# Kernel optimization log

Measured on AMD Instinct MI355X. Metric: run time of the kernel, lower is better.

Reference implementation:

```python
import jax, jax.numpy as jnp
import numpy as np

EPS = 1e-5  # BatchNorm eps; fresh module eval => running_mean=0, running_var=1


def _cbr(t, W, g, b):
    # 1x1 conv (no bias) over [B,C,L] + BatchNorm2d(eval, mean0/var1) + ReLU
    t = jnp.einsum('oc,bcl->bol', W, t)
    t = t * (g / jnp.sqrt(1.0 + EPS))[None, :, None] + b[None, :, None]
    return jax.nn.relu(t)


def _wavelet(y):
    # SFP.wavelet: chunk channels into 3; for chunk i (1-based) take the level-i
    # haar wavedec approximation coeffs along axis 2 and mean-reduce them.
    # For even lengths, level-i haar approx = block-sum over 2^i samples * 2^(-i/2).
    B, C, L = y.shape
    parts = jnp.split(y, 3, axis=1)
    zs = []
    for i, k in enumerate(parts, start=1):
        s = 2 ** i
        a = k.reshape(B, C // 3, L // s, s).sum(-1) * (2.0 ** (-i / 2))  # [B,C/3,L/2^i]
        zs.append(a.mean(axis=2))
    return jnp.concatenate(zs, axis=1)  # [B,C]


def setup_inputs() -> dict:
    key = jax.random.key(0)
    ks = jax.random.split(key, 16)
    B, C, H, W = 32, 384, 64, 64
    R = C // 16
    f = lambda k, sh, s=0.05: jax.random.normal(k, sh, jnp.float32) * s
    u = lambda k, sh: jax.random.uniform(k, sh, jnp.float32, 0.5, 1.5)
    return dict(
        x=jax.random.normal(ks[0], (B, C, H, W), jnp.float32),
        Wy=f(ks[1], (C, C)), gy=u(ks[2], (C,)), by=f(ks[3], (C,)),
        Wh=f(ks[4], (C, C)), gh=u(ks[5], (C,)), bh=f(ks[6], (C,)),
        Ww=f(ks[7], (C, C)), gw=u(ks[8], (C,)), bw=f(ks[9], (C,)),
        fc0_w=f(ks[10], (R, C)), fc0_b=f(ks[11], (R,)),
        bn1_g=u(ks[12], (R,)), bn1_b=f(ks[13], (R,)),
        fc1_w=f(ks[14], (C, R)), fc1_b=f(ks[15], (C,)),
    )


def reference(x, Wy, gy, by, Wh, gh, bh, Ww, gw, bw,
              fc0_w, fc0_b, bn1_g, bn1_b, fc1_w, fc1_b):
    B, C, H, Wd = x.shape
    # CoordPooling: mean over width -> [B,C,H]; mean over height -> [B,C,W]; cat along coord axis
    y = jnp.concatenate([x.mean(axis=3), x.mean(axis=2)], axis=2)  # [B,C,H+W]
    y = _cbr(y, Wy, gy, by)
    xh = _cbr(y[:, :, :H], Wh, gh, bh)   # [B,C,H]
    xw = _cbr(y[:, :, H:], Ww, gw, bw)   # [B,C,W]
    # SFP channel gate (torch detaches y before the wavelet)
    z = _wavelet(jax.lax.stop_gradient(y))          # [B,C]
    z = z @ fc0_w.T + fc0_b                          # [B,C/16]
    z = jax.nn.relu(z * (bn1_g / jnp.sqrt(1.0 + EPS)) + bn1_b)
    z = z @ fc1_w.T + fc1_b                          # [B,C]
    gate = jax.nn.sigmoid(xh[:, :, :, None] * xw[:, :, None, :])  # [B,C,H,W]
    return x * gate + x * z[:, :, None, None]
```

## Files before the change

### kernel.cpp

```cpp
#include <hip/hip_runtime.h>
#include <math.h>

#define RSQ 0.99999500003749975f

typedef __attribute__((ext_vector_type(8))) __bf16 bf16x8;
typedef __attribute__((ext_vector_type(4))) float f32x4;
typedef __attribute__((ext_vector_type(4))) unsigned int u32x4;
typedef __attribute__((ext_vector_type(2))) unsigned int u32x2;

__device__ __forceinline__ unsigned short bfb(float v) {
    return __builtin_bit_cast(unsigned short, (__bf16)v);
}
__device__ __forceinline__ float bff(unsigned short u) {
    unsigned int x = ((unsigned int)u) << 16;
    return __builtin_bit_cast(float, x);
}

__global__ __launch_bounds__(256) void kpool(const float* __restrict__ x,
                                             const float* __restrict__ Wy,
                                             const float* __restrict__ Wh,
                                             const float* __restrict__ Ww,
                                             unsigned short* __restrict__ ypb,
                                             unsigned short* __restrict__ Wp) {
    __shared__ float sm[6208];
    int bid = blockIdx.x;
    int t = threadIdx.x;
    if (bid >= 12288) {
        int e = bid - 12288;
        int m = e / 24, ot = e % 24;
        const float* W = (m == 0) ? Wy : (m == 1) ? Wh : Ww;
#pragma unroll
        for (int k = 0; k < 6; ++k) {
            int idx = t + k * 256;
            int r = idx / 96, c4 = idx % 96;
            f32x4 v = *reinterpret_cast<const f32x4*>(W + (size_t)(ot * 16 + r) * 384 + c4 * 4);
            *reinterpret_cast<f32x4*>(&sm[r * 388 + c4 * 4]) = v;
        }
        __syncthreads();
#pragma unroll
        for (int k = 0; k < 3; ++k) {
            int idx = t + k * 256;
            int cs = idx >> 6, j = idx & 63;
            const float* src = &sm[(j & 15) * 388 + cs * 32 + (j >> 4) * 8];
            u32x4 pk;
            pk.x = (unsigned int)bfb(src[0]) | ((unsigned int)bfb(src[1]) << 16);
            pk.y = (unsigned int)bfb(src[2]) | ((unsigned int)bfb(src[3]) << 16);
            pk.z = (unsigned int)bfb(src[4]) | ((unsigned int)bfb(src[5]) << 16);
            pk.w = (unsigned int)bfb(src[6]) | ((unsigned int)bfb(src[7]) << 16);
            *reinterpret_cast<u32x4*>(Wp + ((size_t)(m * 24 + ot) * 12 + cs) * 512 + j * 8) = pk;
        }
        return;
    }
    float* pl = sm;
    float* part = sm + 4096;
    const f32x4* xp = reinterpret_cast<const f32x4*>(x) + (size_t)bid * 1024;
    f32x4* pl4 = reinterpret_cast<f32x4*>(pl);
#pragma unroll
    for (int k = 0; k < 4; ++k) pl4[k * 256 + t] = xp[k * 256 + t];
    __syncthreads();
    int lane = t & 63, pt = t >> 6;
    float rs = 0.f;
#pragma unroll
    for (int j = 0; j < 16; ++j) {
        int w = (pt * 16 + j + lane) & 63;
        rs += pl[lane * 64 + w];
    }
    part[t] = rs;
    __syncthreads();
    if (t < 64) {
        float v = part[t] + part[t + 64] + part[t + 128] + part[t + 192];
        ypb[(size_t)bid * 128 + t] = bfb(v * 0.015625f);
    }
    __syncthreads();
    float cs = 0.f;
#pragma unroll
    for (int j = 0; j < 16; ++j) cs += pl[(pt * 16 + j) * 64 + lane];
    part[t] = cs;
    __syncthreads();
    if (t < 64) {
        float v = part[t] + part[t + 64] + part[t + 128] + part[t + 192];
        ypb[(size_t)bid * 128 + 64 + t] = bfb(v * 0.015625f);
    }
}

__global__ __launch_bounds__(256) void kcbr1(const unsigned short* __restrict__ yp,
    const unsigned short* __restrict__ Wp,
    const float* __restrict__ g, const float* __restrict__ bb,
    unsigned short* __restrict__ yT) {
    __shared__ unsigned short Bs[2][2048];
    int bid = blockIdx.x;
    int t = threadIdx.x;
    int ot = bid % 6, lt = (bid / 6) % 4, b = bid / 24;
    int o0 = ot * 64, l0 = lt * 32;
    int w = t >> 6, lane = t & 63;

    int c_s0 = t >> 3, l4_0 = (t & 7) * 4;
    int c_s1 = (t + 256) >> 3;
    const unsigned short* ypbase = yp + (size_t)b * 49152 + l0;
    const unsigned short* Asrc = Wp + (size_t)(ot * 4 + w) * 12 * 512 + lane * 8;

    f32x4 acc0 = {0.f, 0.f, 0.f, 0.f};
    f32x4 acc1 = {0.f, 0.f, 0.f, 0.f};

    auto stage = [&](int buf, u32x2 r0, u32x2 r1) {
        unsigned short* B0 = &Bs[buf][(c_s0 >> 3) * 256 + l4_0 * 8 + (c_s0 & 7)];
        B0[0] = (unsigned short)(r0.x & 0xffff); B0[8] = (unsigned short)(r0.x >> 16);
        B0[16] = (unsigned short)(r0.y & 0xffff); B0[24] = (unsigned short)(r0.y >> 16);
        unsigned short* B1 = &Bs[buf][(c_s1 >> 3) * 256 + l4_0 * 8 + (c_s1 & 7)];
        B1[0] = (unsigned short)(r1.x & 0xffff); B1[8] = (unsigned short)(r1.x >> 16);
        B1[16] = (unsigned short)(r1.y & 0xffff); B1[24] = (unsigned short)(r1.y >> 16);
    };
    u32x2 r0, r1;
    r0 = *reinterpret_cast<const u32x2*>(ypbase + (size_t)c_s0 * 128 + l4_0);
    r1 = *reinterpret_cast<const u32x2*>(ypbase + (size_t)c_s1 * 128 + l4_0);
    stage(0, r0, r1);
#pragma unroll
    for (int ch = 0; ch < 6; ++ch) {
        __syncthreads();
        if (ch < 5) {
            r0 = *reinterpret_cast<const u32x2*>(ypbase + (size_t)((ch + 1) * 64 + c_s0) * 128 + l4_0);
            r1 = *reinterpret_cast<const u32x2*>(ypbase + (size_t)((ch + 1) * 64 + c_s1) * 128 + l4_0);
        }
        const unsigned short* Bb = Bs[ch & 1];
        int li = lane & 15, hi = lane >> 4;
#pragma unroll
        for (int kk = 0; kk < 2; ++kk) {
            bf16x8 av = *reinterpret_cast<const bf16x8*>(Asrc + (size_t)(ch * 2 + kk) * 512);
            int cg2 = kk * 4 + hi;
            bf16x8 bv0 = *reinterpret_cast<const bf16x8*>(&Bb[cg2 * 256 + li * 8]);
            bf16x8 bv1 = *reinterpret_cast<const bf16x8*>(&Bb[cg2 * 256 + (li + 16) * 8]);
            acc0 = __builtin_amdgcn_mfma_f32_16x16x32_bf16(av, bv0, acc0, 0, 0, 0);
            acc1 = __builtin_amdgcn_mfma_f32_16x16x32_bf16(av, bv1, acc1, 0, 0, 0);
        }
        if (ch < 5) stage((ch + 1) & 1, r0, r1);
    }
    int oB = o0 + w * 16 + (lane >> 4) * 4;
    int lB = l0 + (lane & 15);
    float s0 = g[oB] * RSQ, bi0 = bb[oB];
    float s1 = g[oB + 1] * RSQ, bi1 = bb[oB + 1];
    float s2 = g[oB + 2] * RSQ, bi2 = bb[oB + 2];
    float s3 = g[oB + 3] * RSQ, bi3 = bb[oB + 3];
    u32x2 p0, p1;
    p0.x = (unsigned int)bfb(fmaxf(fmaf(acc0[0], s0, bi0), 0.f)) |
           ((unsigned int)bfb(fmaxf(fmaf(acc0[1], s1, bi1), 0.f)) << 16);
    p0.y = (unsigned int)bfb(fmaxf(fmaf(acc0[2], s2, bi2), 0.f)) |
           ((unsigned int)bfb(fmaxf(fmaf(acc0[3], s3, bi3), 0.f)) << 16);
    p1.x = (unsigned int)bfb(fmaxf(fmaf(acc1[0], s0, bi0), 0.f)) |
           ((unsigned int)bfb(fmaxf(fmaf(acc1[1], s1, bi1), 0.f)) << 16);
    p1.y = (unsigned int)bfb(fmaxf(fmaf(acc1[2], s2, bi2), 0.f)) |
           ((unsigned int)bfb(fmaxf(fmaf(acc1[3], s3, bi3), 0.f)) << 16);
    *reinterpret_cast<u32x2*>(yT + ((size_t)b * 128 + lB) * 384 + oB) = p0;
    *reinterpret_cast<u32x2*>(yT + ((size_t)b * 128 + lB + 16) * 384 + oB) = p1;
}

__global__ __launch_bounds__(256, 3) void kcbr2(const unsigned short* __restrict__ yT,
    const unsigned short* __restrict__ Wp,
    const float* __restrict__ gh, const float* __restrict__ bh,
    const float* __restrict__ gw, const float* __restrict__ bw,
    float* __restrict__ hw,
    const float* __restrict__ fc0_w, const float* __restrict__ fc0_b,
    const float* __restrict__ bn1_g, const float* __restrict__ bn1_b,
    const float* __restrict__ fc1_w, const float* __restrict__ fc1_b,
    float* __restrict__ z2) {
    int bid = blockIdx.x;
    int t = threadIdx.x;
    if (bid >= 768) {
        __shared__ float z0[384];
        __shared__ float z1[24];
        int b = bid - 768;
        const unsigned short* yb = yT + (size_t)b * 49152;
        if (t < 192) {
            int c2 = t * 2;
            float s0 = 0.f, s1 = 0.f;
#pragma unroll 8
            for (int l = 0; l < 128; ++l) {
                unsigned int v = *reinterpret_cast<const unsigned int*>(yb + (size_t)l * 384 + c2);
                s0 += bff((unsigned short)(v & 0xffff));
                s1 += bff((unsigned short)(v >> 16));
            }
            float fac = (c2 < 128) ? 1.41421356237310f : (c2 < 256 ? 2.0f : 2.82842712474619f);
            z0[c2]     = s0 * (fac * 0.0078125f);
            z0[c2 + 1] = s1 * (fac * 0.0078125f);
        }
        __syncthreads();
        if (t < 96) {
            int r = t >> 2, j = t & 3;
            float p = 0.f;
            for (int c = j; c < 384; c += 4) p = fmaf(z0[c], fc0_w[r * 384 + c], p);
            p += __shfl_xor(p, 1);
            p += __shfl_xor(p, 2);
            if (j == 0) z1[r] = fmaxf(fmaf(p + fc0_b[r], bn1_g[r] * RSQ, bn1_b[r]), 0.f);
        }
        __syncthreads();
        for (int c = t; c < 384; c += 256) {
            float a = fc1_b[c];
#pragma unroll
            for (int r = 0; r < 24; ++r) a = fmaf(z1[r], fc1_w[c * 24 + r], a);
            z2[b * 384 + c] = a;
        }
        return;
    }
    int ot = bid % 6, lt = (bid / 6) % 4, b = bid / 24;
    int o0 = ot * 64, l0 = lt * 32;
    int m = (lt >= 2) ? 2 : 1;
    const float* g  = (lt >= 2) ? gw : gh;
    const float* bb = (lt >= 2) ? bw : bh;
    int w = t >> 6, lane = t & 63;
    int li = lane & 15, hi = lane >> 4;
    const unsigned short* Asrc = Wp + (size_t)(m * 24 + ot * 4 + w) * 12 * 512 + lane * 8;
    const unsigned short* B0 = yT + ((size_t)b * 128 + l0 + li) * 384 + hi * 8;
    const unsigned short* B1 = B0 + (size_t)16 * 384;

    f32x4 acc0 = {0.f, 0.f, 0.f, 0.f};
    f32x4 acc1 = {0.f, 0.f, 0.f, 0.f};
    bf16x8 av  = *reinterpret_cast<const bf16x8*>(Asrc);
    bf16x8 bv0 = *reinterpret_cast<const bf16x8*>(B0);
    bf16x8 bv1 = *reinterpret_cast<const bf16x8*>(B1);
    for (int ch = 0; ch < 12; ++ch) {
        bf16x8 avn, bv0n, bv1n;
        if (ch < 11) {
            avn  = *reinterpret_cast<const bf16x8*>(Asrc + (size_t)(ch + 1) * 512);
            bv0n = *reinterpret_cast<const bf16x8*>(B0 + (ch + 1) * 32);
            bv1n = *reinterpret_cast<const bf16x8*>(B1 + (ch + 1) * 32);
        }
        acc0 = __builtin_amdgcn_mfma_f32_16x16x32_bf16(av, bv0, acc0, 0, 0, 0);
        acc1 = __builtin_amdgcn_mfma_f32_16x16x32_bf16(av, bv1, acc1, 0, 0, 0);
        av = avn; bv0 = bv0n; bv1 = bv1n;
    }
    int oB = o0 + w * 16 + hi * 4;
    int lB = l0 + li;
#pragma unroll
    for (int r = 0; r < 4; ++r) {
        int o = oB + r;
        float sc = g[o] * RSQ, bi = bb[o];
        size_t base = ((size_t)b * 384 + o) * 128 + lB;
        hw[base]      = fmaxf(fmaf(acc0[r], sc, bi), 0.f);
        hw[base + 16] = fmaxf(fmaf(acc1[r], sc, bi), 0.f);
    }
}

__global__ __launch_bounds__(256) void kfinal(const float* __restrict__ x,
    const float* __restrict__ hw, const float* __restrict__ z2,
    float* __restrict__ out) {
    const f32x4* x4 = reinterpret_cast<const f32x4*>(x);
    f32x4* o4 = reinterpret_cast<f32x4*>(out);
    const int total4 = 12582912;
    int stride = gridDim.x * blockDim.x;
    for (int idx = blockIdx.x * blockDim.x + threadIdx.x; idx < total4; idx += stride) {
        int w4 = idx & 15;
        int h  = (idx >> 4) & 63;
        int bc = idx >> 10;
        f32x4 xv = x4[idx];
        float  a  = hw[(bc << 7) + h];
        const f32x4 wv = reinterpret_cast<const f32x4*>(hw)[(bc << 5) + 16 + w4];
        float  zv = z2[bc];
        f32x4 ov;
        ov.x = xv.x * (1.f / (1.f + __expf(-a * wv.x)) + zv);
        ov.y = xv.y * (1.f / (1.f + __expf(-a * wv.y)) + zv);
        ov.z = xv.z * (1.f / (1.f + __expf(-a * wv.z)) + zv);
        ov.w = xv.w * (1.f / (1.f + __expf(-a * wv.w)) + zv);
        __builtin_nontemporal_store(ov, o4 + idx);
    }
}

extern "C" void kernel_launch(void* const* d_in, const int* in_sizes, int n_in,
                              void* d_out, int out_size, void* d_ws, size_t ws_size,
                              hipStream_t stream) {
    const float* x     = (const float*)d_in[0];
    const float* Wy    = (const float*)d_in[1];
    const float* gy    = (const float*)d_in[2];
    const float* by    = (const float*)d_in[3];
    const float* Wh    = (const float*)d_in[4];
    const float* gh    = (const float*)d_in[5];
    const float* bh    = (const float*)d_in[6];
    const float* Ww    = (const float*)d_in[7];
    const float* gw    = (const float*)d_in[8];
    const float* bw    = (const float*)d_in[9];
    const float* fc0_w = (const float*)d_in[10];
    const float* fc0_b = (const float*)d_in[11];
    const float* bn1_g = (const float*)d_in[12];
    const float* bn1_b = (const float*)d_in[13];
    const float* fc1_w = (const float*)d_in[14];
    const float* fc1_b = (const float*)d_in[15];
    float* out = (float*)d_out;

    char* ws = (char*)d_ws;
    unsigned short* ypb = (unsigned short*)ws;
    unsigned short* yT  = (unsigned short*)(ws + 3145728);
    float*          hww = (float*)(ws + 6291456);
    float*          z2  = (float*)(ws + 12582912);
    unsigned short* Wp  = (unsigned short*)(ws + 12632064);

    kpool<<<dim3(12288 + 72), dim3(256), 0, stream>>>(x, Wy, Wh, Ww, ypb, Wp);
    kcbr1<<<dim3(768), dim3(256), 0, stream>>>(ypb, Wp, gy, by, yT);
    kcbr2<<<dim3(800), dim3(256), 0, stream>>>(yT, Wp, gh, bh, gw, bw, hww,
        fc0_w, fc0_b, bn1_g, bn1_b, fc1_w, fc1_b, z2);
    kfinal<<<dim3(2048), dim3(256), 0, stream>>>(x, hww, z2, out);
}
```

Before: 126.7 us.

## Store pooled features transposed so conv1 reads MFMA operands directly from global

Measured after the change: 134.3 us. 6.1% more time.

```diff
diff --git a/kernel.cpp b/kernel.cpp
--- a/kernel.cpp
+++ b/kernel.cpp
@@ -20,9 +20,9 @@
                                              const float* __restrict__ Wy,
                                              const float* __restrict__ Wh,
                                              const float* __restrict__ Ww,
-                                             unsigned short* __restrict__ ypb,
+                                             unsigned short* __restrict__ ypT,
                                              unsigned short* __restrict__ Wp) {
-    __shared__ float sm[6208];
+    __shared__ float sm[4352];
     int bid = blockIdx.x;
     int t = threadIdx.x;
     if (bid >= 12288) {
@@ -30,24 +30,33 @@
         int m = e / 24, ot = e % 24;
         const float* W = (m == 0) ? Wy : (m == 1) ? Wh : Ww;
 #pragma unroll
-        for (int k = 0; k < 6; ++k) {
-            int idx = t + k * 256;
-            int r = idx / 96, c4 = idx % 96;
-            f32x4 v = *reinterpret_cast<const f32x4*>(W + (size_t)(ot * 16 + r) * 384 + c4 * 4);
-            *reinterpret_cast<f32x4*>(&sm[r * 388 + c4 * 4]) = v;
-        }
-        __syncthreads();
-#pragma unroll
-        for (int k = 0; k < 3; ++k) {
-            int idx = t + k * 256;
-            int cs = idx >> 6, j = idx & 63;
-            const float* src = &sm[(j & 15) * 388 + cs * 32 + (j >> 4) * 8];
-            u32x4 pk;
-            pk.x = (unsigned int)bfb(src[0]) | ((unsigned int)bfb(src[1]) << 16);
-            pk.y = (unsigned int)bfb(src[2]) | ((unsigned int)bfb(src[3]) << 16);
-            pk.z = (unsigned int)bfb(src[4]) | ((unsigned int)bfb(src[5]) << 16);
-            pk.w = (unsigned int)bfb(src[6]) | ((unsigned int)bfb(src[7]) << 16);
-            *reinterpret_cast<u32x4*>(Wp + ((size_t)(m * 24 + ot) * 12 + cs) * 512 + j * 8) = pk;
+        for (int half = 0; half < 2; ++half) {
+            if (half) __syncthreads();
+#pragma unroll
+            for (int k = 0; k < 3; ++k) {
+                int idx = t + k * 256;
+                int r = idx / 48, c4 = idx % 48;
+                f32x4 v = *reinterpret_cast<const f32x4*>(
+                    W + (size_t)(ot * 16 + r) * 384 + half * 192 + c4 * 4);
+                *reinterpret_cast<f32x4*>(&sm[r * 196 + c4 * 4]) = v;
+            }
+            __syncthreads();
+#pragma unroll
+            for (int k = 0; k < 2; ++k) {
+                int idx = t + k * 256;
+                if (idx < 384) {
+                    int cs_l = idx >> 6, j = idx & 63;
+                    const float* src = &sm[(j & 15) * 196 + cs_l * 32 + (j >> 4) * 8];
+                    u32x4 pk;
+                    pk.x = (unsigned int)bfb(src[0]) | ((unsigned int)bfb(src[1]) << 16);
+                    pk.y = (unsigned int)bfb(src[2]) | ((unsigned int)bfb(src[3]) << 16);
+                    pk.z = (unsigned int)bfb(src[4]) | ((unsigned int)bfb(src[5]) << 16);
+                    pk.w = (unsigned int)bfb(src[6]) | ((unsigned int)bfb(src[7]) << 16);
+                    int cs = half * 6 + cs_l;
+                    *reinterpret_cast<u32x4*>(
+                        Wp + ((size_t)(m * 24 + ot) * 12 + cs) * 512 + j * 8) = pk;
+                }
+            }
         }
         return;
     }
@@ -59,6 +68,8 @@
     for (int k = 0; k < 4; ++k) pl4[k * 256 + t] = xp[k * 256 + t];
     __syncthreads();
     int lane = t & 63, pt = t >> 6;
+    int b = bid / 384, c = bid % 384;
+    unsigned short* ypb = ypT + (size_t)b * 49152 + c;
     float rs = 0.f;
 #pragma unroll
     for (int j = 0; j < 16; ++j) {
@@ -69,7 +80,7 @@
     __syncthreads();
     if (t < 64) {
         float v = part[t] + part[t + 64] + part[t + 128] + part[t + 192];
-        ypb[(size_t)bid * 128 + t] = bfb(v * 0.015625f);
+        ypb[(size_t)t * 384] = bfb(v * 0.015625f);
     }
     __syncthreads();
     float cs = 0.f;
@@ -79,63 +90,42 @@
     __syncthreads();
     if (t < 64) {
         float v = part[t] + part[t + 64] + part[t + 128] + part[t + 192];
-        ypb[(size_t)bid * 128 + 64 + t] = bfb(v * 0.015625f);
-    }
-}
-
-__global__ __launch_bounds__(256) void kcbr1(const unsigned short* __restrict__ yp,
+        ypb[(size_t)(64 + t) * 384] = bfb(v * 0.015625f);
+    }
+}
+
+__global__ __launch_bounds__(256, 3) void kcbr1(const unsigned short* __restrict__ ypT,
     const unsigned short* __restrict__ Wp,
     const float* __restrict__ g, const float* __restrict__ bb,
     unsigned short* __restrict__ yT) {
-    __shared__ unsigned short Bs[2][2048];
     int bid = blockIdx.x;
     int t = threadIdx.x;
     int ot = bid % 6, lt = (bid / 6) % 4, b = bid / 24;
     int o0 = ot * 64, l0 = lt * 32;
     int w = t >> 6, lane = t & 63;
-
-    int c_s0 = t >> 3, l4_0 = (t & 7) * 4;
-    int c_s1 = (t + 256) >> 3;
-    const unsigned short* ypbase = yp + (size_t)b * 49152 + l0;
+    int li = lane & 15, hi = lane >> 4;
     const unsigned short* Asrc = Wp + (size_t)(ot * 4 + w) * 12 * 512 + lane * 8;
+    const unsigned short* B0 = ypT + ((size_t)b * 128 + l0 + li) * 384 + hi * 8;
+    const unsigned short* B1 = B0 + (size_t)16 * 384;
 
     f32x4 acc0 = {0.f, 0.f, 0.f, 0.f};
     f32x4 acc1 = {0.f, 0.f, 0.f, 0.f};
-
-    auto stage = [&](int buf, u32x2 r0, u32x2 r1) {
-        unsigned short* B0 = &Bs[buf][(c_s0 >> 3) * 256 + l4_0 * 8 + (c_s0 & 7)];
-        B0[0] = (unsigned short)(r0.x & 0xffff); B0[8] = (unsigned short)(r0.x >> 16);
-        B0[16] = (unsigned short)(r0.y & 0xffff); B0[24] = (unsigned short)(r0.y >> 16);
-        unsigned short* B1 = &Bs[buf][(c_s1 >> 3) * 256 + l4_0 * 8 + (c_s1 & 7)];
-        B1[0] = (unsigned short)(r1.x & 0xffff); B1[8] = (unsigned short)(r1.x >> 16);
-        B1[16] = (unsigned short)(r1.y & 0xffff); B1[24] = (unsigned short)(r1.y >> 16);
-    };
-    u32x2 r0, r1;
-    r0 = *reinterpret_cast<const u32x2*>(ypbase + (size_t)c_s0 * 128 + l4_0);
-    r1 = *reinterpret_cast<const u32x2*>(ypbase + (size_t)c_s1 * 128 + l4_0);
-    stage(0, r0, r1);
-#pragma unroll
-    for (int ch = 0; ch < 6; ++ch) {
-        __syncthreads();
-        if (ch < 5) {
-            r0 = *reinterpret_cast<const u32x2*>(ypbase + (size_t)((ch + 1) * 64 + c_s0) * 128 + l4_0);
-            r1 = *reinterpret_cast<const u32x2*>(ypbase + (size_t)((ch + 1) * 64 + c_s1) * 128 + l4_0);
-        }
-        const unsigned short* Bb = Bs[ch & 1];
-        int li = lane & 15, hi = lane >> 4;
-#pragma unroll
-        for (int kk = 0; kk < 2; ++kk) {
-            bf16x8 av = *reinterpret_cast<const bf16x8*>(Asrc + (size_t)(ch * 2 + kk) * 512);
-            int cg2 = kk * 4 + hi;
-            bf16x8 bv0 = *reinterpret_cast<const bf16x8*>(&Bb[cg2 * 256 + li * 8]);
-            bf16x8 bv1 = *reinterpret_cast<const bf16x8*>(&Bb[cg2 * 256 + (li + 16) * 8]);
-            acc0 = __builtin_amdgcn_mfma_f32_16x16x32_bf16(av, bv0, acc0, 0, 0, 0);
-            acc1 = __builtin_amdgcn_mfma_f32_16x16x32_bf16(av, bv1, acc1, 0, 0, 0);
-        }
-        if (ch < 5) stage((ch + 1) & 1, r0, r1);
-    }
-    int oB = o0 + w * 16 + (lane >> 4) * 4;
-    int lB = l0 + (lane & 15);
+    bf16x8 av  = *reinterpret_cast<const bf16x8*>(Asrc);
+    bf16x8 bv0 = *reinterpret_cast<const bf16x8*>(B0);
+    bf16x8 bv1 = *reinterpret_cast<const bf16x8*>(B1);
+    for (int ch = 0; ch < 12; ++ch) {
+        bf16x8 avn, bv0n, bv1n;
+        if (ch < 11) {
+            avn  = *reinterpret_cast<const bf16x8*>(Asrc + (size_t)(ch + 1) * 512);
+            bv0n = *reinterpret_cast<const bf16x8*>(B0 + (ch + 1) * 32);
+            bv1n = *reinterpret_cast<const bf16x8*>(B1 + (ch + 1) * 32);
+        }
+        acc0 = __builtin_amdgcn_mfma_f32_16x16x32_bf16(av, bv0, acc0, 0, 0, 0);
+        acc1 = __builtin_amdgcn_mfma_f32_16x16x32_bf16(av, bv1, acc1, 0, 0, 0);
+        av = avn; bv0 = bv0n; bv1 = bv1n;
+    }
+    int oB = o0 + w * 16 + hi * 4;
+    int lB = l0 + li;
     float s0 = g[oB] * RSQ, bi0 = bb[oB];
     float s1 = g[oB + 1] * RSQ, bi1 = bb[oB + 1];
     float s2 = g[oB + 2] * RSQ, bi2 = bb[oB + 2];
@@ -285,14 +275,14 @@
     float* out = (float*)d_out;
 
     char* ws = (char*)d_ws;
-    unsigned short* ypb = (unsigned short*)ws;
+    unsigned short* ypT = (unsigned short*)ws;
     unsigned short* yT  = (unsigned short*)(ws + 3145728);
     float*          hww = (float*)(ws + 6291456);
     float*          z2  = (float*)(ws + 12582912);
     unsigned short* Wp  = (unsigned short*)(ws + 12632064);
 
-    kpool<<<dim3(12288 + 72), dim3(256), 0, stream>>>(x, Wy, Wh, Ww, ypb, Wp);
-    kcbr1<<<dim3(768), dim3(256), 0, stream>>>(ypb, Wp, gy, by, yT);
+    kpool<<<dim3(12288 + 72), dim3(256), 0, stream>>>(x, Wy, Wh, Ww, ypT, Wp);
+    kcbr1<<<dim3(768), dim3(256), 0, stream>>>(ypT, Wp, gy, by, yT);
     kcbr2<<<dim3(800), dim3(256), 0, stream>>>(yT, Wp, gh, bh, gw, bw, hww,
         fc0_w, fc0_b, bn1_g, bn1_b, fc1_w, fc1_b, z2);
     kfinal<<<dim3(2048), dim3(256), 0, stream>>>(x, hww, z2, out);
```
